# Performance work log

Measured on AMD Instinct MI355X. Metric: run time of the kernel, lower is better.

Reference implementation:

```python
import jax, jax.numpy as jnp
import numpy as np

B = 2048      # seed nodes per batch
F1, F2 = 10, 25  # fanouts
D = 128       # combined dense feature dim
H = 256       # hidden_dim
N = 1 + F1 + F1 * F2  # 261 hop-ordered sampled nodes per seed


def setup_inputs() -> dict:
    key = jax.random.key(0)
    k1, k2, k3 = jax.random.split(key, 3)
    x = jax.random.normal(k1, (B, N, D), dtype=jnp.float32)
    W1 = jax.random.normal(k2, (2 * D, H), dtype=jnp.float32) / np.sqrt(2.0 * D)
    b1 = jnp.zeros((H,), dtype=jnp.float32)
    W2 = jax.random.normal(k3, (2 * H, H), dtype=jnp.float32) / np.sqrt(2.0 * H)
    b2 = jnp.zeros((H,), dtype=jnp.float32)
    return {"x": x, "W1": W1, "b1": b1, "W2": W2, "b2": b2}


def _sage(src, neigh_mean, W, b):
    # concat(self, mean(neighbors)) -> dense : GraphSAGE mean aggregator
    return jnp.concatenate([src, neigh_mean], axis=-1) @ W + b


def reference(x, W1, b1, W2, b2):
    # split hop-ordered flat features into bipartite blocks
    seeds = x[:, :1, :]                         # [B, 1, D]   hop0
    hop1 = x[:, 1:1 + F1, :]                    # [B, F1, D]  hop1
    hop2 = x[:, 1 + F1:, :].reshape(B, F1, F2, D)  # [B, F1, F2, D] hop2

    # SAGE layer 1 (relu): update hop0 and hop1 nodes
    h0 = jax.nn.relu(_sage(seeds, jnp.mean(hop1, axis=1, keepdims=True), W1, b1))  # [B, 1, H]
    h1 = jax.nn.relu(_sage(hop1, jnp.mean(hop2, axis=2), W1, b1))                  # [B, F1, H]

    # SAGE layer 2 (no activation): update hop0 from hop1
    out = _sage(h0, jnp.mean(h1, axis=1, keepdims=True), W2, b2)  # [B, 1, H]
    # matches tf.squeeze(src_feature [B,1,1,H], axis=2) -> [B, 1, H]
    return out
```

## Files before the change

### kernel.cpp

```cpp
#include <hip/hip_runtime.h>


#define NB 2048
#define F1 10
#define F2 25
#define DD 128
#define HH 256
#define NN 261
#define ITEMS 4
#define THREADS 256

typedef __attribute__((ext_vector_type(8))) short short8;
typedef __attribute__((ext_vector_type(4))) float f32x4;

__device__ __forceinline__ ushort f2bf(float f) {
    unsigned u = __builtin_bit_cast(unsigned, f);
    u = (u + 0x7FFFu + ((u >> 16) & 1u)) >> 16;
    return (ushort)u;
}
__device__ __forceinline__ float bf2f(ushort h) {
    unsigned u = ((unsigned)h) << 16;
    return __builtin_bit_cast(float, u);
}
__device__ __forceinline__ int swz(int uidx, int row) {
    return uidx ^ ((row & 7) << 3);
}

__global__ __launch_bounds__(256)
void prep_weights(const float* __restrict__ W1, const float* __restrict__ W2,
                  ushort* __restrict__ W1t, ushort* __restrict__ W2t)
{
    __shared__ float tile[32][257];
    const int b = blockIdx.x, t = threadIdx.x;
    const float* src; ushort* dst; int K, c0, k0;
    if (b < 8) { src = W1; dst = W1t; K = 2 * DD; c0 = b * 32; k0 = 0; }
    else { int bb = b - 8; src = W2; dst = W2t; K = 2 * HH;
           c0 = (bb & 7) * 32; k0 = (bb >> 3) * 256; }

    #pragma unroll 4
    for (int kr = 0; kr < 32; ++kr) {
        int kl = kr * 8 + (t >> 5);
        tile[t & 31][kl] = src[(size_t)(k0 + kl) * HH + c0 + (t & 31)];
    }
    __syncthreads();
    const int cl = t >> 3;
    #pragma unroll
    for (int p = 0; p < 4; ++p) {
        int kc = (t & 7) + p * 8;
        short8 v;
        #pragma unroll
        for (int i = 0; i < 8; ++i) v[i] = (short)f2bf(tile[cl][kc * 8 + i]);
        *reinterpret_cast<short8*>(dst + (size_t)(c0 + cl) * K + k0 + kc * 8) = v;
    }
}

__global__ __launch_bounds__(THREADS)
void sage_fused(const float* __restrict__ x, const ushort* __restrict__ W1t,
                const ushort* __restrict__ W2t, const float* __restrict__ b1,
                const float* __restrict__ b2, float* __restrict__ out)
{
    __shared__ ushort featL[ITEMS * 16 * 256];
    __shared__ ushort f2lds[16][520];

    const int t = threadIdx.x;
    const int item0 = blockIdx.x * ITEMS;
    const size_t base = (size_t)item0 * (NN * DD);

    {
        const int g = t >> 5, d4 = t & 31;
        #pragma unroll
        for (int p = 0; p < 5; ++p) {
            int pi = g + p * 8;
            int item = pi / 10, f = pi % 10;
            const float4* xb = reinterpret_cast<const float4*>(x + base + (size_t)item * (NN * DD));
            float4 h1 = xb[(1 + f) * 32 + d4];
            float4 s = make_float4(0.f, 0.f, 0.f, 0.f);
            const float4* h2 = xb + (1 + F1 + f * F2) * 32 + d4;
            #pragma unroll 5
            for (int j = 0; j < F2; ++j) {
                float4 v = h2[j * 32];
                s.x += v.x; s.y += v.y; s.z += v.z; s.w += v.w;
            }
            const float invF2 = 1.f / F2;
            int row = 1 + f;
            int ub = (item * 16 + row) * 256;
            ushort4 lo = { f2bf(h1.x), f2bf(h1.y), f2bf(h1.z), f2bf(h1.w) };
            ushort4 hi = { f2bf(s.x * invF2), f2bf(s.y * invF2),
                           f2bf(s.z * invF2), f2bf(s.w * invF2) };
            *reinterpret_cast<ushort4*>(&featL[swz(ub + d4 * 4, row)]) = lo;
            *reinterpret_cast<ushort4*>(&featL[swz(ub + DD + d4 * 4, row)]) = hi;
        }
    }
    __syncthreads();

    #pragma unroll
    for (int q = 0; q < 2; ++q) {
        int idx = t + q * 256;
        int item = idx >> 7, d = idx & 127;
        int r0 = item * 16 * 256;
        float sv = x[base + (size_t)item * (NN * DD) + d];
        featL[swz(r0 + d, 0)] = f2bf(sv);
        float m = 0.f;
        #pragma unroll
        for (int f = 1; f <= F1; ++f) m += bf2f(featL[swz(r0 + f * 256 + d, f)]);
        featL[swz(r0 + DD + d, 0)] = f2bf(m * (1.f / F1));
    }
    {
        short8 zz = { 0, 0, 0, 0, 0, 0, 0, 0 };
        for (int z = t; z < ITEMS * 5 * 32; z += THREADS) {
            int item = z / 160, rem = z % 160;
            int row = 11 + rem / 32, kc = rem % 32;
            *reinterpret_cast<short8*>(&featL[swz((item * 16 + row) * 256 + kc * 8, row)]) = zz;
        }
        for (int z = t; z < 12 * 64; z += THREADS) {
            int row = ITEMS + (z >> 6), kc = z & 63;
            *reinterpret_cast<short8*>(&f2lds[row][kc * 8]) = zz;
        }
    }
    __syncthreads();

    const int w = t >> 6, l = t & 63;
    const int lr = l & 15, lg = l >> 4;
    f32x4 acc[ITEMS][4];
    #pragma unroll
    for (int it = 0; it < ITEMS; ++it)
        #pragma unroll
        for (int i = 0; i < 4; ++i) acc[it][i] = (f32x4){0.f, 0.f, 0.f, 0.f};

    #pragma unroll 2
    for (int kt = 0; kt < 8; ++kt) {
        short8 af[ITEMS], bf[4];
        #pragma unroll
        for (int it = 0; it < ITEMS; ++it)
            af[it] = *reinterpret_cast<const short8*>(
                &featL[swz((it * 16 + lr) * 256 + kt * 32 + lg * 8, lr)]);
        #pragma unroll
        for (int i = 0; i < 4; ++i) {
            int col = (w * 4 + i) * 16 + lr;
            bf[i] = *reinterpret_cast<const short8*>(W1t + (size_t)col * 256 + kt * 32 + lg * 8);
        }
        #pragma unroll
        for (int it = 0; it < ITEMS; ++it)
            #pragma unroll
            for (int i = 0; i < 4; ++i)
                acc[it][i] = __builtin_amdgcn_mfma_f32_16x16x32_bf16(af[it], bf[i], acc[it][i], 0, 0, 0);
    }

    #pragma unroll
    for (int i = 0; i < 4; ++i) {
        const int col = (w * 4 + i) * 16 + lr;
        const float bb = b1[col];
        #pragma unroll
        for (int it = 0; it < ITEMS; ++it) {
            f32x4 a = acc[it][i];
            float r0v = fmaxf(a[0] + bb, 0.f);
            float r1v = fmaxf(a[1] + bb, 0.f);
            float r2v = fmaxf(a[2] + bb, 0.f);
            float r3v = fmaxf(a[3] + bb, 0.f);
            const int rb = lg * 4;
            float p = 0.f;
            p += (rb + 0 >= 1 && rb + 0 <= 10) ? r0v : 0.f;
            p += (rb + 1 >= 1 && rb + 1 <= 10) ? r1v : 0.f;
            p += (rb + 2 >= 1 && rb + 2 <= 10) ? r2v : 0.f;
            p += (rb + 3 >= 1 && rb + 3 <= 10) ? r3v : 0.f;
            p += __shfl_xor(p, 16, 64);
            p += __shfl_xor(p, 32, 64);
            if (lg == 0) {
                f2lds[it][col]       = f2bf(r0v);
                f2lds[it][256 + col] = f2bf(p * (1.f / F1));
            }
        }
    }
    __syncthreads();

    f32x4 acc2[4];
    #pragma unroll
    for (int i = 0; i < 4; ++i) acc2[i] = (f32x4){0.f, 0.f, 0.f, 0.f};
    #pragma unroll 2
    for (int kt = 0; kt < 16; ++kt) {
        short8 a2 = *reinterpret_cast<const short8*>(&f2lds[lr][kt * 32 + lg * 8]);
        #pragma unroll
        for (int i = 0; i < 4; ++i) {
            int col = (w * 4 + i) * 16 + lr;
            short8 bv = *reinterpret_cast<const short8*>(W2t + (size_t)col * 512 + kt * 32 + lg * 8);
            acc2[i] = __builtin_amdgcn_mfma_f32_16x16x32_bf16(a2, bv, acc2[i], 0, 0, 0);
        }
    }
    #pragma unroll
    for (int i = 0; i < 4; ++i) {
        const int col = (w * 4 + i) * 16 + lr;
        const float bb = b2[col];
        #pragma unroll
        for (int r = 0; r < 4; ++r) {
            const int row = lg * 4 + r;
            if (row < ITEMS)
                out[(size_t)(item0 + row) * HH + col] = acc2[i][r] + bb;
        }
    }
}

extern "C" void kernel_launch(void* const* d_in, const int* in_sizes, int n_in,
                              void* d_out, int out_size, void* d_ws, size_t ws_size,
                              hipStream_t stream) {
    const float* x  = (const float*)d_in[0];
    const float* W1 = (const float*)d_in[1];
    const float* b1 = (const float*)d_in[2];
    const float* W2 = (const float*)d_in[3];
    const float* b2 = (const float*)d_in[4];
    float* out = (float*)d_out;

    ushort* W1t = (ushort*)d_ws;
    ushort* W2t = W1t + 256 * 256;

    prep_weights<<<dim3(24), dim3(256), 0, stream>>>(W1, W2, W1t, W2t);
    sage_fused<<<dim3(NB / ITEMS), dim3(THREADS), 0, stream>>>(x, W1t, W2t, b1, b2, out);
}
```

Baseline: 75.60 us.

## Halve items per block, split hop2 reduction across half-waves, widen weight prep grid

Items per block drop from 4 to 2, doubling the grid to 1024 blocks, and a launch-bounds minimum of 4 blocks per CU is added. Each wave now handles 5 (item, fanout) pairs and splits the 25-row hop2 sum between two half-waves, combining them with a cross-lane shuffle. The x reads use nontemporal loads. The weight transpose kernel now runs on 96 smaller tiles, which spreads the prep work over more CUs. The aim is more memory-level parallelism for streaming x, at the cost of reloading each weight fragment for fewer items per block.

```diff
diff --git a/kernel.cpp b/kernel.cpp
--- a/kernel.cpp
+++ b/kernel.cpp
@@ -7,11 +7,12 @@
 #define DD 128
 #define HH 256
 #define NN 261
-#define ITEMS 4
+#define ITEMS 2
 #define THREADS 256
 
 typedef __attribute__((ext_vector_type(8))) short short8;
 typedef __attribute__((ext_vector_type(4))) float f32x4;
+typedef __attribute__((ext_vector_type(4))) float vf4;
 
 __device__ __forceinline__ ushort f2bf(float f) {
     unsigned u = __builtin_bit_cast(unsigned, f);
@@ -30,31 +31,28 @@
 void prep_weights(const float* __restrict__ W1, const float* __restrict__ W2,
                   ushort* __restrict__ W1t, ushort* __restrict__ W2t)
 {
-    __shared__ float tile[32][257];
+    __shared__ float tile[32][65];
     const int b = blockIdx.x, t = threadIdx.x;
     const float* src; ushort* dst; int K, c0, k0;
-    if (b < 8) { src = W1; dst = W1t; K = 2 * DD; c0 = b * 32; k0 = 0; }
-    else { int bb = b - 8; src = W2; dst = W2t; K = 2 * HH;
-           c0 = (bb & 7) * 32; k0 = (bb >> 3) * 256; }
-
-    #pragma unroll 4
-    for (int kr = 0; kr < 32; ++kr) {
+    if (b < 32) { src = W1; dst = W1t; K = 2 * DD;
+                  c0 = (b & 7) * 32; k0 = (b >> 3) * 64; }
+    else { int bb = b - 32; src = W2; dst = W2t; K = 2 * HH;
+           c0 = (bb & 7) * 32; k0 = (bb >> 3) * 64; }
+
+    #pragma unroll
+    for (int kr = 0; kr < 8; ++kr) {
         int kl = kr * 8 + (t >> 5);
         tile[t & 31][kl] = src[(size_t)(k0 + kl) * HH + c0 + (t & 31)];
     }
     __syncthreads();
-    const int cl = t >> 3;
-    #pragma unroll
-    for (int p = 0; p < 4; ++p) {
-        int kc = (t & 7) + p * 8;
-        short8 v;
-        #pragma unroll
-        for (int i = 0; i < 8; ++i) v[i] = (short)f2bf(tile[cl][kc * 8 + i]);
-        *reinterpret_cast<short8*>(dst + (size_t)(c0 + cl) * K + k0 + kc * 8) = v;
-    }
-}
-
-__global__ __launch_bounds__(THREADS)
+    const int cl = t >> 3, kc = t & 7;
+    short8 v;
+    #pragma unroll
+    for (int i = 0; i < 8; ++i) v[i] = (short)f2bf(tile[cl][kc * 8 + i]);
+    *reinterpret_cast<short8*>(dst + (size_t)(c0 + cl) * K + k0 + kc * 8) = v;
+}
+
+__global__ __launch_bounds__(THREADS, 4)
 void sage_fused(const float* __restrict__ x, const ushort* __restrict__ W1t,
                 const ushort* __restrict__ W2t, const float* __restrict__ b1,
                 const float* __restrict__ b2, float* __restrict__ out)
@@ -63,42 +61,52 @@
     __shared__ ushort f2lds[16][520];
 
     const int t = threadIdx.x;
+    const int w = t >> 6, l = t & 63;
     const int item0 = blockIdx.x * ITEMS;
-    const size_t base = (size_t)item0 * (NN * DD);
 
     {
-        const int g = t >> 5, d4 = t & 31;
-        #pragma unroll
-        for (int p = 0; p < 5; ++p) {
-            int pi = g + p * 8;
-            int item = pi / 10, f = pi % 10;
-            const float4* xb = reinterpret_cast<const float4*>(x + base + (size_t)item * (NN * DD));
-            float4 h1 = xb[(1 + f) * 32 + d4];
-            float4 s = make_float4(0.f, 0.f, 0.f, 0.f);
-            const float4* h2 = xb + (1 + F1 + f * F2) * 32 + d4;
-            #pragma unroll 5
-            for (int j = 0; j < F2; ++j) {
-                float4 v = h2[j * 32];
-                s.x += v.x; s.y += v.y; s.z += v.z; s.w += v.w;
+        const int d4 = l & 31, jh = l >> 5;
+        #pragma unroll
+        for (int q = 0; q < 5; ++q) {
+            const int pair = w * 5 + q;
+            const int item = pair / 10, f = pair % 10;
+            const vf4* xb = reinterpret_cast<const vf4*>(x)
+                          + (size_t)(item0 + item) * (NN * DD / 4);
+            const vf4* h2 = xb + (1 + F1 + f * F2) * 32 + d4;
+            vf4 s = (vf4){0.f, 0.f, 0.f, 0.f};
+            const int j0 = jh * 12;
+            #pragma unroll
+            for (int j = 0; j < 12; ++j)
+                s += __builtin_nontemporal_load(&h2[(j0 + j) * 32]);
+            vf4 h1 = (vf4){0.f, 0.f, 0.f, 0.f};
+            if (jh == 0) {
+                h1 = __builtin_nontemporal_load(&xb[(1 + f) * 32 + d4]);
+            } else {
+                s += __builtin_nontemporal_load(&h2[24 * 32]);
             }
-            const float invF2 = 1.f / F2;
-            int row = 1 + f;
-            int ub = (item * 16 + row) * 256;
-            ushort4 lo = { f2bf(h1.x), f2bf(h1.y), f2bf(h1.z), f2bf(h1.w) };
-            ushort4 hi = { f2bf(s.x * invF2), f2bf(s.y * invF2),
-                           f2bf(s.z * invF2), f2bf(s.w * invF2) };
-            *reinterpret_cast<ushort4*>(&featL[swz(ub + d4 * 4, row)]) = lo;
-            *reinterpret_cast<ushort4*>(&featL[swz(ub + DD + d4 * 4, row)]) = hi;
-        }
-    }
-    __syncthreads();
-
-    #pragma unroll
-    for (int q = 0; q < 2; ++q) {
-        int idx = t + q * 256;
-        int item = idx >> 7, d = idx & 127;
-        int r0 = item * 16 * 256;
-        float sv = x[base + (size_t)item * (NN * DD) + d];
+            s.x += __shfl_xor(s.x, 32, 64);
+            s.y += __shfl_xor(s.y, 32, 64);
+            s.z += __shfl_xor(s.z, 32, 64);
+            s.w += __shfl_xor(s.w, 32, 64);
+            const int row = 1 + f;
+            const int ub = (item * 16 + row) * 256;
+            if (jh == 0) {
+                ushort4 lo = { f2bf(h1.x), f2bf(h1.y), f2bf(h1.z), f2bf(h1.w) };
+                *reinterpret_cast<ushort4*>(&featL[swz(ub + d4 * 4, row)]) = lo;
+            } else {
+                const float inv = 1.f / F2;
+                ushort4 hi = { f2bf(s.x * inv), f2bf(s.y * inv),
+                               f2bf(s.z * inv), f2bf(s.w * inv) };
+                *reinterpret_cast<ushort4*>(&featL[swz(ub + DD + d4 * 4, row)]) = hi;
+            }
+        }
+    }
+    __syncthreads();
+
+    {
+        const int item = t >> 7, d = t & 127;
+        const int r0 = item * 16 * 256;
+        float sv = x[(size_t)(item0 + item) * (NN * DD) + d];
         featL[swz(r0 + d, 0)] = f2bf(sv);
         float m = 0.f;
         #pragma unroll
@@ -112,14 +120,13 @@
             int row = 11 + rem / 32, kc = rem % 32;
             *reinterpret_cast<short8*>(&featL[swz((item * 16 + row) * 256 + kc * 8, row)]) = zz;
         }
-        for (int z = t; z < 12 * 64; z += THREADS) {
+        for (int z = t; z < (16 - ITEMS) * 64; z += THREADS) {
             int row = ITEMS + (z >> 6), kc = z & 63;
             *reinterpret_cast<short8*>(&f2lds[row][kc * 8]) = zz;
         }
     }
     __syncthreads();
 
-    const int w = t >> 6, l = t & 63;
     const int lr = l & 15, lg = l >> 4;
     f32x4 acc[ITEMS][4];
     #pragma unroll
@@ -212,6 +219,6 @@
     ushort* W1t = (ushort*)d_ws;
     ushort* W2t = W1t + 256 * 256;
 
-    prep_weights<<<dim3(24), dim3(256), 0, stream>>>(W1, W2, W1t, W2t);
+    prep_weights<<<dim3(96), dim3(256), 0, stream>>>(W1, W2, W1t, W2t);
     sage_fused<<<dim3(NB / ITEMS), dim3(THREADS), 0, stream>>>(x, W1t, W2t, b1, b2, out);
 }
```

Measured after the change: 90.45 us. +19.6%, slower.
